# Kernel tuning notes

Measured on AMD Instinct MI355X. Metric: run time of the kernel, lower is better.

Reference implementation:

```python
import jax, jax.numpy as jnp
import numpy as np

TEMPERATURE = 8.0  # sqrt(dim_k=64)
NEG_INF = -1e30    # stand-in for -inf that stays finite-safe under softmax


def setup_inputs() -> dict:
    key = jax.random.key(0)
    kq, kk, kv, km = jax.random.split(key, 4)
    bsz, lq, lk, d = 64, 2048, 2048, 64
    q = jax.random.normal(kq, (bsz, lq, d), dtype=jnp.float32)
    k = jax.random.normal(kk, (bsz, lk, d), dtype=jnp.float32)
    v = jax.random.normal(kv, (bsz, lk, d), dtype=jnp.float32)
    mask = jax.random.normal(km, (bsz, lq, lk), dtype=jnp.float32)
    return {"q": q, "k": k, "v": v, "mask": mask}


def reference(q, k, v, mask):
    # attn = QK^T / temperature, additive graph mask, threshold -inf fill
    attn = jnp.einsum("bqd,bkd->bqk", q, k) / TEMPERATURE
    attn = attn + mask                       # graph_mask_type == 'add'
    attn = jnp.where(mask < 0, NEG_INF, attn)  # masked_fill(mask.lt(0), -inf)
    attn = jax.nn.softmax(attn, axis=2)
    # dropout p=0.0 -> identity
    output = jnp.einsum("bqk,bkd->bqd", attn, v)
    return (output, attn)
```

## Files before the change

kernel.cpp:

```cpp
#include <hip/hip_runtime.h>
#include <stdint.h>
#include <stddef.h>


typedef __attribute__((ext_vector_type(4))) float f32x4;
typedef __fp16 f16x2 __attribute__((ext_vector_type(2)));
typedef __fp16 f16x4 __attribute__((ext_vector_type(4)));
typedef __fp16 f16x8 __attribute__((ext_vector_type(8)));

static constexpr int BATCH = 64;
static constexpr int SEQ   = 2048;
static constexpr int HD    = 64;
static constexpr float NEGH = -60000.0f;

__global__ void frag_kernel(const float* __restrict__ k, const float* __restrict__ v,
                            __fp16* __restrict__ kf, __fp16* __restrict__ vf) {
  __shared__ float tile[64][68];
  if (blockIdx.x < 2048) {
    const int b    = blockIdx.x >> 5;
    const int ch   = blockIdx.x & 31;
    const int tid  = threadIdx.x;
    const int tl   = tid >> 6;
    const int lane = tid & 63;
    const int l15  = lane & 15;
    const int g    = lane >> 4;
    const int kt   = ch * 4 + tl;
    const float* src = k + ((size_t)(b * SEQ + kt * 16 + l15)) * HD + g * 8;
    char* dst = (char*)kf + ((size_t)(b * 128 + kt)) * 2048 + l15 * 64 + g * 16;
#pragma unroll
    for (int half = 0; half < 2; ++half) {
      f32x4 a = *(const f32x4*)(src + half * 32);
      f32x4 c = *(const f32x4*)(src + half * 32 + 4);
      f16x2 p0 = __builtin_amdgcn_cvt_pkrtz(a[0], a[1]);
      f16x2 p1 = __builtin_amdgcn_cvt_pkrtz(a[2], a[3]);
      f16x2 p2 = __builtin_amdgcn_cvt_pkrtz(c[0], c[1]);
      f16x2 p3 = __builtin_amdgcn_cvt_pkrtz(c[2], c[3]);
      f16x8 o;
      o[0] = p0[0]; o[1] = p0[1]; o[2] = p1[0]; o[3] = p1[1];
      o[4] = p2[0]; o[5] = p2[1]; o[6] = p3[0]; o[7] = p3[1];
      *(f16x8*)(dst + half * 1024) = o;
    }
  } else {
    const int bid = blockIdx.x - 2048;
    const int b   = bid >> 5;
    const int ch  = bid & 31;
    const int tid = threadIdx.x;
    const int kk  = tid >> 4;
    const int d4  = (tid & 15) << 2;
    const int k0  = ch * 64;
#pragma unroll
    for (int i = 0; i < 4; ++i) {
      f32x4 val = *(const f32x4*)(v + ((size_t)(b * SEQ + k0 + kk + 16 * i)) * HD + d4);
      tile[kk + 16 * i][d4 + 0] = val[0];
      tile[kk + 16 * i][d4 + 1] = val[1];
      tile[kk + 16 * i][d4 + 2] = val[2];
      tile[kk + 16 * i][d4 + 3] = val[3];
    }
    __syncthreads();
    const int tl  = tid >> 6;
    const int db  = (tid >> 4) & 3;
    const int l15 = tid & 15;
    f16x8 o0, o1;
#pragma unroll
    for (int g = 0; g < 2; ++g)
#pragma unroll
      for (int j = 0; j < 4; ++j)
        o0[g * 4 + j] = (__fp16)tile[tl * 16 + g * 4 + j][db * 16 + l15];
#pragma unroll
    for (int g = 0; g < 2; ++g)
#pragma unroll
      for (int j = 0; j < 4; ++j)
        o1[g * 4 + j] = (__fp16)tile[tl * 16 + (g + 2) * 4 + j][db * 16 + l15];
    char* dst = (char*)vf + ((size_t)(b * 128 + ch * 4 + tl)) * 2048 + db * 512 + l15 * 32;
    *(f16x8*)(dst)      = o0;
    *(f16x8*)(dst + 16) = o1;
  }
}

__global__ __launch_bounds__(256, 3) void attn_kernel(
    const float* __restrict__ q,
    const __fp16* __restrict__ kf,
    const __fp16* __restrict__ vf,
    const float* __restrict__ mask,
    float* __restrict__ out,
    float* __restrict__ attn) {
  __shared__ __align__(16) char pool[4][4352];
  __shared__ float stat_m[4][16];
  __shared__ float stat_l[4][16];

  const int tid  = threadIdx.x;
  const int w    = tid >> 6;
  const int lane = tid & 63;
  const int l15  = lane & 15;
  const int g    = lane >> 4;
  const int g4   = g << 2;

  const int bid = blockIdx.x;
  const int xcd = bid & 7;
  const int r   = bid >> 3;
  const int b   = xcd * 8 + (r >> 7);
  const int q0  = (r & 127) << 4;
  const int wk0 = w << 9;

  char* wb = pool[w];
  const int koff = l15 * 64 + g * 16;
  const int voff = l15 * 32 + g * 8;

  const char* kfb = (const char*)kf + ((size_t)(b * 128) + w * 32) * 2048;
  const char* vfb = (const char*)vf + ((size_t)(b * 128) + w * 32) * 2048;
  const float* mbase = mask + ((size_t)(b * SEQ + q0)) * SEQ + wk0;
  float*       abase = attn + ((size_t)(b * SEQ + q0)) * SEQ + wk0;

  f16x8 qb0, qb1;
  {
    const float* qsrc = q + ((size_t)(b * SEQ + q0 + l15)) * HD + g * 8;
    f32x4 a0 = *(const f32x4*)(qsrc);
    f32x4 a1 = *(const f32x4*)(qsrc + 4);
    f32x4 c0 = *(const f32x4*)(qsrc + 32);
    f32x4 c1 = *(const f32x4*)(qsrc + 36);
    f16x2 p0 = __builtin_amdgcn_cvt_pkrtz(a0[0], a0[1]);
    f16x2 p1 = __builtin_amdgcn_cvt_pkrtz(a0[2], a0[3]);
    f16x2 p2 = __builtin_amdgcn_cvt_pkrtz(a1[0], a1[1]);
    f16x2 p3 = __builtin_amdgcn_cvt_pkrtz(a1[2], a1[3]);
    qb0[0] = p0[0]; qb0[1] = p0[1]; qb0[2] = p1[0]; qb0[3] = p1[1];
    qb0[4] = p2[0]; qb0[5] = p2[1]; qb0[6] = p3[0]; qb0[7] = p3[1];
    p0 = __builtin_amdgcn_cvt_pkrtz(c0[0], c0[1]);
    p1 = __builtin_amdgcn_cvt_pkrtz(c0[2], c0[3]);
    p2 = __builtin_amdgcn_cvt_pkrtz(c1[0], c1[1]);
    p3 = __builtin_amdgcn_cvt_pkrtz(c1[2], c1[3]);
    qb1[0] = p0[0]; qb1[1] = p0[1]; qb1[2] = p1[0]; qb1[3] = p1[1];
    qb1[4] = p2[0]; qb1[5] = p2[1]; qb1[6] = p3[0]; qb1[7] = p3[1];
  }

  f16x4 PH0,  PH1,  PH2,  PH3,  PH4,  PH5,  PH6,  PH7;
  f16x4 PH8,  PH9,  PH10, PH11, PH12, PH13, PH14, PH15;
  f16x4 PH16, PH17, PH18, PH19, PH20, PH21, PH22, PH23;
  f16x4 PH24, PH25, PH26, PH27, PH28, PH29, PH30, PH31;

  f16x8 K0A, K0B, K1A, K1B, K2A, K2B, K3A, K3B;
  f32x4 MA0, MA1, MA2, MA3;
  f32x4 MB0, MB1, MB2, MB3;
  float m = -3.0e38f;

#define ISSUE_K(t, KA, KB)                                                   \
  KA = *(const f16x8*)(kfb + (size_t)(t) * 2048 + koff);                     \
  KB = *(const f16x8*)(kfb + (size_t)(t) * 2048 + 1024 + koff);

#define ISSUE_M(c, M0, M1, M2, M3)                                           \
  M0 = __builtin_nontemporal_load((const f32x4*)(mbase + (size_t)(0 * 4 + g) * SEQ + (c) * 64 + l15 * 4)); \
  M1 = __builtin_nontemporal_load((const f32x4*)(mbase + (size_t)(1 * 4 + g) * SEQ + (c) * 64 + l15 * 4)); \
  M2 = __builtin_nontemporal_load((const f32x4*)(mbase + (size_t)(2 * 4 + g) * SEQ + (c) * 64 + l15 * 4)); \
  M3 = __builtin_nontemporal_load((const f32x4*)(mbase + (size_t)(3 * 4 + g) * SEQ + (c) * 64 + l15 * 4));

#define WRITE_M(M0, M1, M2, M3)                                              \
  *(f32x4*)(wb + (0 * 4 + g) * 272 + l15 * 16) = M0;                         \
  *(f32x4*)(wb + (1 * 4 + g) * 272 + l15 * 16) = M1;                         \
  *(f32x4*)(wb + (2 * 4 + g) * 272 + l15 * 16) = M2;                         \
  *(f32x4*)(wb + (3 * 4 + g) * 272 + l15 * 16) = M3;

#define ATILE(t, PH, KA, KB)                                                 \
  {                                                                          \
    f32x4 acc = {0.f, 0.f, 0.f, 0.f};                                        \
    acc = __builtin_amdgcn_mfma_f32_16x16x32_f16(KA, qb0, acc, 0, 0, 0);     \
    acc = __builtin_amdgcn_mfma_f32_16x16x32_f16(KB, qb1, acc, 0, 0, 0);     \
    const f32x4 mv = *(const f32x4*)(wb + l15 * 272 + ((t) & 3) * 64 + g * 16); \
    float s0 = (mv[0] < 0.f) ? NEGH : fmaf(acc[0], 0.125f, mv[0]);           \
    float s1 = (mv[1] < 0.f) ? NEGH : fmaf(acc[1], 0.125f, mv[1]);           \
    float s2 = (mv[2] < 0.f) ? NEGH : fmaf(acc[2], 0.125f, mv[2]);           \
    float s3 = (mv[3] < 0.f) ? NEGH : fmaf(acc[3], 0.125f, mv[3]);           \
    m = fmaxf(m, fmaxf(fmaxf(s0, s1), fmaxf(s2, s3)));                       \
    f16x2 lo_ = __builtin_amdgcn_cvt_pkrtz(s0, s1);                          \
    f16x2 hi_ = __builtin_amdgcn_cvt_pkrtz(s2, s3);                          \
    PH = (f16x4){lo_[0], lo_[1], hi_[0], hi_[1]};                            \
  }

#define AT(t, PH, KA, KB)  ATILE(t, PH, KA, KB) ISSUE_K((t) + 4, KA, KB)
#define ATL(t, PH, KA, KB) ATILE(t, PH, KA, KB)

  ISSUE_M(0, MA0, MA1, MA2, MA3)
  ISSUE_K(0, K0A, K0B) ISSUE_K(1, K1A, K1B) ISSUE_K(2, K2A, K2B) ISSUE_K(3, K3A, K3B)
  ISSUE_M(1, MB0, MB1, MB2, MB3)

  WRITE_M(MA0, MA1, MA2, MA3) ISSUE_M(2, MA0, MA1, MA2, MA3)
  AT(0, PH0, K0A, K0B)  AT(1, PH1, K1A, K1B)  AT(2, PH2, K2A, K2B)  AT(3, PH3, K3A, K3B)
  WRITE_M(MB0, MB1, MB2, MB3) ISSUE_M(3, MB0, MB1, MB2, MB3)
  AT(4, PH4, K0A, K0B)  AT(5, PH5, K1A, K1B)  AT(6, PH6, K2A, K2B)  AT(7, PH7, K3A, K3B)
  WRITE_M(MA0, MA1, MA2, MA3) ISSUE_M(4, MA0, MA1, MA2, MA3)
  AT(8, PH8, K0A, K0B)  AT(9, PH9, K1A, K1B)  AT(10, PH10, K2A, K2B) AT(11, PH11, K3A, K3B)
  WRITE_M(MB0, MB1, MB2, MB3) ISSUE_M(5, MB0, MB1, MB2, MB3)
  AT(12, PH12, K0A, K0B) AT(13, PH13, K1A, K1B) AT(14, PH14, K2A, K2B) AT(15, PH15, K3A, K3B)
  WRITE_M(MA0, MA1, MA2, MA3) ISSUE_M(6, MA0, MA1, MA2, MA3)
  AT(16, PH16, K0A, K0B) AT(17, PH17, K1A, K1B) AT(18, PH18, K2A, K2B) AT(19, PH19, K3A, K3B)
  WRITE_M(MB0, MB1, MB2, MB3) ISSUE_M(7, MB0, MB1, MB2, MB3)
  AT(20, PH20, K0A, K0B) AT(21, PH21, K1A, K1B) AT(22, PH22, K2A, K2B) AT(23, PH23, K3A, K3B)
  WRITE_M(MA0, MA1, MA2, MA3)
  AT(24, PH24, K0A, K0B) AT(25, PH25, K1A, K1B) AT(26, PH26, K2A, K2B) AT(27, PH27, K3A, K3B)
  WRITE_M(MB0, MB1, MB2, MB3)
  ATL(28, PH28, K0A, K0B) ATL(29, PH29, K1A, K1B) ATL(30, PH30, K2A, K2B) ATL(31, PH31, K3A, K3B)

#undef AT
#undef ATL
#undef ATILE
#undef ISSUE_K
#undef ISSUE_M
#undef WRITE_M

  m = fmaxf(m, __shfl_xor(m, 16));
  m = fmaxf(m, __shfl_xor(m, 32));

  float lw = 0.f;
#define A2_STEP(PH)                                                          \
  {                                                                          \
    float e0 = __expf((float)PH[0] - m);                                     \
    float e1 = __expf((float)PH[1] - m);                                     \
    float e2 = __expf((float)PH[2] - m);                                     \
    float e3 = __expf((float)PH[3] - m);                                     \
    lw += (e0 + e1) + (e2 + e3);                                             \
    f16x2 lo_ = __builtin_amdgcn_cvt_pkrtz(e0, e1);                          \
    f16x2 hi_ = __builtin_amdgcn_cvt_pkrtz(e2, e3);                          \
    PH = (f16x4){lo_[0], lo_[1], hi_[0], hi_[1]};                            \
  }
  A2_STEP(PH0)  A2_STEP(PH1)  A2_STEP(PH2)  A2_STEP(PH3)
  A2_STEP(PH4)  A2_STEP(PH5)  A2_STEP(PH6)  A2_STEP(PH7)
  A2_STEP(PH8)  A2_STEP(PH9)  A2_STEP(PH10) A2_STEP(PH11)
  A2_STEP(PH12) A2_STEP(PH13) A2_STEP(PH14) A2_STEP(PH15)
  A2_STEP(PH16) A2_STEP(PH17) A2_STEP(PH18) A2_STEP(PH19)
  A2_STEP(PH20) A2_STEP(PH21) A2_STEP(PH22) A2_STEP(PH23)
  A2_STEP(PH24) A2_STEP(PH25) A2_STEP(PH26) A2_STEP(PH27)
  A2_STEP(PH28) A2_STEP(PH29) A2_STEP(PH30) A2_STEP(PH31)
#undef A2_STEP

  lw += __shfl_xor(lw, 16);
  lw += __shfl_xor(lw, 32);

  if (lane < 16) { stat_m[w][lane] = m; stat_l[w][lane] = lw; }
  __syncthreads();

  float mg = -3.0e38f;
#pragma unroll
  for (int ww = 0; ww < 4; ++ww) mg = fmaxf(mg, stat_m[ww][l15]);
  float lg = 0.f;
#pragma unroll
  for (int ww = 0; ww < 4; ++ww) lg += stat_l[ww][l15] * __expf(stat_m[ww][l15] - mg);
  const float scale = __expf(m - mg) / lg;
  const __fp16 hs = (__fp16)scale;
  const f16x4 sc4 = {hs, hs, hs, hs};

  f32x4 oacc0 = {0.f, 0.f, 0.f, 0.f};
  f32x4 oacc1 = {0.f, 0.f, 0.f, 0.f};
  f32x4 oacc2 = {0.f, 0.f, 0.f, 0.f};
  f32x4 oacc3 = {0.f, 0.f, 0.f, 0.f};

  f16x4 V0a, V0b, V0c, V0d, V1a, V1b, V1c, V1d;
  f16x4 V2a, V2b, V2c, V2d, V3a, V3b, V3c, V3d;

#define ISSUE_V(t, Va, Vb, Vc, Vd)                                           \
  Va = *(const f16x4*)(vfb + (size_t)(t) * 2048 + 0 * 512 + voff);           \
  Vb = *(const f16x4*)(vfb + (size_t)(t) * 2048 + 1 * 512 + voff);           \
  Vc = *(const f16x4*)(vfb + (size_t)(t) * 2048 + 2 * 512 + voff);           \
  Vd = *(const f16x4*)(vfb + (size_t)(t) * 2048 + 3 * 512 + voff);

#define BTILE(t, PH, Va, Vb, Vc, Vd)                                         \
  {                                                                          \
    const f16x4 pf = PH * sc4;                                               \
    f32x4 st;                                                                \
    st[0] = (float)pf[0]; st[1] = (float)pf[1];                              \
    st[2] = (float)pf[2]; st[3] = (float)pf[3];                              \
    *(f32x4*)(wb + l15 * 272 + ((t) & 3) * 64 + g * 16) = st;                \
    oacc0 = __builtin_amdgcn_mfma_f32_16x16x16f16(Va, pf, oacc0, 0, 0, 0);   \
    oacc1 = __builtin_amdgcn_mfma_f32_16x16x16f16(Vb, pf, oacc1, 0, 0, 0);   \
    oacc2 = __builtin_amdgcn_mfma_f32_16x16x16f16(Vc, pf, oacc2, 0, 0, 0);   \
    oacc3 = __builtin_amdgcn_mfma_f32_16x16x16f16(Vd, pf, oacc3, 0, 0, 0);   \
  }

#define STORE_A(c)                                                           \
  __builtin_nontemporal_store(                                               \
      *(const f32x4*)(wb + (0 * 4 + g) * 272 + l15 * 16),                    \
      (f32x4*)(abase + (size_t)(0 * 4 + g) * SEQ + (c) * 64 + l15 * 4));     \
  __builtin_nontemporal_store(                                               \
      *(const f32x4*)(wb + (1 * 4 + g) * 272 + l15 * 16),                    \
      (f32x4*)(abase + (size_t)(1 * 4 + g) * SEQ + (c) * 64 + l15 * 4));     \
  __builtin_nontemporal_store(                                               \
      *(const f32x4*)(wb + (2 * 4 + g) * 272 + l15 * 16),                    \
      (f32x4*)(abase + (size_t)(2 * 4 + g) * SEQ + (c) * 64 + l15 * 4));     \
  __builtin_nontemporal_store(                                               \
      *(const f32x4*)(wb + (3 * 4 + g) * 272 + l15 * 16),                    \
      (f32x4*)(abase + (size_t)(3 * 4 + g) * SEQ + (c) * 64 + l15 * 4));

#define BS(t, PH, Va, Vb, Vc, Vd)  BTILE(t, PH, Va, Vb, Vc, Vd) ISSUE_V((t) + 4, Va, Vb, Vc, Vd)
#define BSL(t, PH, Va, Vb, Vc, Vd) BTILE(t, PH, Va, Vb, Vc, Vd)

  ISSUE_V(0, V0a, V0b, V0c, V0d) ISSUE_V(1, V1a, V1b, V1c, V1d)
  ISSUE_V(2, V2a, V2b, V2c, V2d) ISSUE_V(3, V3a, V3b, V3c, V3d)

  BS(0, PH0, V0a, V0b, V0c, V0d)   BS(1, PH1, V1a, V1b, V1c, V1d)
  BS(2, PH2, V2a, V2b, V2c, V2d)   BS(3, PH3, V3a, V3b, V3c, V3d)   STORE_A(0)
  BS(4, PH4, V0a, V0b, V0c, V0d)   BS(5, PH5, V1a, V1b, V1c, V1d)
  BS(6, PH6, V2a, V2b, V2c, V2d)   BS(7, PH7, V3a, V3b, V3c, V3d)   STORE_A(1)
  BS(8, PH8, V0a, V0b, V0c, V0d)   BS(9, PH9, V1a, V1b, V1c, V1d)
  BS(10, PH10, V2a, V2b, V2c, V2d) BS(11, PH11, V3a, V3b, V3c, V3d) STORE_A(2)
  BS(12, PH12, V0a, V0b, V0c, V0d) BS(13, PH13, V1a, V1b, V1c, V1d)
  BS(14, PH14, V2a, V2b, V2c, V2d) BS(15, PH15, V3a, V3b, V3c, V3d) STORE_A(3)
  BS(16, PH16, V0a, V0b, V0c, V0d) BS(17, PH17, V1a, V1b, V1c, V1d)
  BS(18, PH18, V2a, V2b, V2c, V2d) BS(19, PH19, V3a, V3b, V3c, V3d) STORE_A(4)
  BS(20, PH20, V0a, V0b, V0c, V0d) BS(21, PH21, V1a, V1b, V1c, V1d)
  BS(22, PH22, V2a, V2b, V2c, V2d) BS(23, PH23, V3a, V3b, V3c, V3d) STORE_A(5)
  BS(24, PH24, V0a, V0b, V0c, V0d) BS(25, PH25, V1a, V1b, V1c, V1d)
  BS(26, PH26, V2a, V2b, V2c, V2d) BS(27, PH27, V3a, V3b, V3c, V3d) STORE_A(6)
  BSL(28, PH28, V0a, V0b, V0c, V0d) BSL(29, PH29, V1a, V1b, V1c, V1d)
  BSL(30, PH30, V2a, V2b, V2c, V2d) BSL(31, PH31, V3a, V3b, V3c, V3d) STORE_A(7)

#undef BS
#undef BSL
#undef BTILE
#undef ISSUE_V
#undef STORE_A

  float* sred_w = (float*)pool[w];
#pragma unroll
  for (int rr = 0; rr < 4; ++rr) {
    sred_w[(0 * 16 + g4 + rr) * 17 + l15] = oacc0[rr];
    sred_w[(1 * 16 + g4 + rr) * 17 + l15] = oacc1[rr];
    sred_w[(2 * 16 + g4 + rr) * 17 + l15] = oacc2[rr];
    sred_w[(3 * 16 + g4 + rr) * 17 + l15] = oacc3[rr];
  }
  __syncthreads();

#pragma unroll
  for (int ii = 0; ii < 4; ++ii) {
    const int i = tid + ii * 256;
    const int qq = i >> 6;
    const int d = i & 63;
    const int o = d * 17 + qq;
    float s = ((const float*)pool[0])[o] + ((const float*)pool[1])[o] +
              ((const float*)pool[2])[o] + ((const float*)pool[3])[o];
    out[((size_t)(b * SEQ + q0 + qq)) * HD + d] = s;
  }
}

extern "C" void kernel_launch(void* const* d_in, const int* in_sizes, int n_in,
                              void* d_out, int out_size, void* d_ws, size_t ws_size,
                              hipStream_t stream) {
  const float* q    = (const float*)d_in[0];
  const float* k    = (const float*)d_in[1];
  const float* v    = (const float*)d_in[2];
  const float* mask = (const float*)d_in[3];

  float* out  = (float*)d_out;
  float* attn = out + (size_t)BATCH * SEQ * HD;

  const size_t nqk = (size_t)BATCH * SEQ * HD;
  __fp16* kfrag = (__fp16*)d_ws;
  __fp16* vfrag = kfrag + nqk;

  frag_kernel<<<dim3(2 * BATCH * 32), dim3(256), 0, stream>>>(k, v, kfrag, vfrag);
  attn_kernel<<<dim3(BATCH * (SEQ / 16)), dim3(256), 0, stream>>>(q, kfrag, vfrag, mask, out, attn);
}
```

Before: 518.5 us.

## Split key dimension across eight waves per block instead of four

Doubles the block to 512 threads so each of eight waves handles 256 keys instead of 512. Per-wave register tiles (PH arrays) are halved, which lowers register pressure and lets more waves run per CU (launch bounds 512,4). In exchange the cross-wave softmax statistics and output reduction span eight partitions, and each wave's mask/K/V prefetch pipeline is shorter, giving less latency hiding per wave.

```diff
diff --git a/kernel.cpp b/kernel.cpp
--- a/kernel.cpp
+++ b/kernel.cpp
@@ -77,16 +77,16 @@
   }
 }
 
-__global__ __launch_bounds__(256, 3) void attn_kernel(
+__global__ __launch_bounds__(512, 4) void attn_kernel(
     const float* __restrict__ q,
     const __fp16* __restrict__ kf,
     const __fp16* __restrict__ vf,
     const float* __restrict__ mask,
     float* __restrict__ out,
     float* __restrict__ attn) {
-  __shared__ __align__(16) char pool[4][4352];
-  __shared__ float stat_m[4][16];
-  __shared__ float stat_l[4][16];
+  __shared__ __align__(16) char pool[8][4352];
+  __shared__ float stat_m[8][16];
+  __shared__ float stat_l[8][16];
 
   const int tid  = threadIdx.x;
   const int w    = tid >> 6;
@@ -100,14 +100,14 @@
   const int r   = bid >> 3;
   const int b   = xcd * 8 + (r >> 7);
   const int q0  = (r & 127) << 4;
-  const int wk0 = w << 9;
+  const int wk0 = w << 8;
 
   char* wb = pool[w];
   const int koff = l15 * 64 + g * 16;
   const int voff = l15 * 32 + g * 8;
 
-  const char* kfb = (const char*)kf + ((size_t)(b * 128) + w * 32) * 2048;
-  const char* vfb = (const char*)vf + ((size_t)(b * 128) + w * 32) * 2048;
+  const char* kfb = (const char*)kf + ((size_t)(b * 128) + w * 16) * 2048;
+  const char* vfb = (const char*)vf + ((size_t)(b * 128) + w * 16) * 2048;
   const float* mbase = mask + ((size_t)(b * SEQ + q0)) * SEQ + wk0;
   float*       abase = attn + ((size_t)(b * SEQ + q0)) * SEQ + wk0;
 
@@ -134,8 +134,6 @@
 
   f16x4 PH0,  PH1,  PH2,  PH3,  PH4,  PH5,  PH6,  PH7;
   f16x4 PH8,  PH9,  PH10, PH11, PH12, PH13, PH14, PH15;
-  f16x4 PH16, PH17, PH18, PH19, PH20, PH21, PH22, PH23;
-  f16x4 PH24, PH25, PH26, PH27, PH28, PH29, PH30, PH31;
 
   f16x8 K0A, K0B, K1A, K1B, K2A, K2B, K3A, K3B;
   f32x4 MA0, MA1, MA2, MA3;
@@ -185,18 +183,10 @@
   AT(0, PH0, K0A, K0B)  AT(1, PH1, K1A, K1B)  AT(2, PH2, K2A, K2B)  AT(3, PH3, K3A, K3B)
   WRITE_M(MB0, MB1, MB2, MB3) ISSUE_M(3, MB0, MB1, MB2, MB3)
   AT(4, PH4, K0A, K0B)  AT(5, PH5, K1A, K1B)  AT(6, PH6, K2A, K2B)  AT(7, PH7, K3A, K3B)
-  WRITE_M(MA0, MA1, MA2, MA3) ISSUE_M(4, MA0, MA1, MA2, MA3)
+  WRITE_M(MA0, MA1, MA2, MA3)
   AT(8, PH8, K0A, K0B)  AT(9, PH9, K1A, K1B)  AT(10, PH10, K2A, K2B) AT(11, PH11, K3A, K3B)
-  WRITE_M(MB0, MB1, MB2, MB3) ISSUE_M(5, MB0, MB1, MB2, MB3)
-  AT(12, PH12, K0A, K0B) AT(13, PH13, K1A, K1B) AT(14, PH14, K2A, K2B) AT(15, PH15, K3A, K3B)
-  WRITE_M(MA0, MA1, MA2, MA3) ISSUE_M(6, MA0, MA1, MA2, MA3)
-  AT(16, PH16, K0A, K0B) AT(17, PH17, K1A, K1B) AT(18, PH18, K2A, K2B) AT(19, PH19, K3A, K3B)
-  WRITE_M(MB0, MB1, MB2, MB3) ISSUE_M(7, MB0, MB1, MB2, MB3)
-  AT(20, PH20, K0A, K0B) AT(21, PH21, K1A, K1B) AT(22, PH22, K2A, K2B) AT(23, PH23, K3A, K3B)
-  WRITE_M(MA0, MA1, MA2, MA3)
-  AT(24, PH24, K0A, K0B) AT(25, PH25, K1A, K1B) AT(26, PH26, K2A, K2B) AT(27, PH27, K3A, K3B)
   WRITE_M(MB0, MB1, MB2, MB3)
-  ATL(28, PH28, K0A, K0B) ATL(29, PH29, K1A, K1B) ATL(30, PH30, K2A, K2B) ATL(31, PH31, K3A, K3B)
+  ATL(12, PH12, K0A, K0B) ATL(13, PH13, K1A, K1B) ATL(14, PH14, K2A, K2B) ATL(15, PH15, K3A, K3B)
 
 #undef AT
 #undef ATL
@@ -224,10 +214,6 @@
   A2_STEP(PH4)  A2_STEP(PH5)  A2_STEP(PH6)  A2_STEP(PH7)
   A2_STEP(PH8)  A2_STEP(PH9)  A2_STEP(PH10) A2_STEP(PH11)
   A2_STEP(PH12) A2_STEP(PH13) A2_STEP(PH14) A2_STEP(PH15)
-  A2_STEP(PH16) A2_STEP(PH17) A2_STEP(PH18) A2_STEP(PH19)
-  A2_STEP(PH20) A2_STEP(PH21) A2_STEP(PH22) A2_STEP(PH23)
-  A2_STEP(PH24) A2_STEP(PH25) A2_STEP(PH26) A2_STEP(PH27)
-  A2_STEP(PH28) A2_STEP(PH29) A2_STEP(PH30) A2_STEP(PH31)
 #undef A2_STEP
 
   lw += __shfl_xor(lw, 16);
@@ -238,10 +224,10 @@
 
   float mg = -3.0e38f;
 #pragma unroll
-  for (int ww = 0; ww < 4; ++ww) mg = fmaxf(mg, stat_m[ww][l15]);
+  for (int ww = 0; ww < 8; ++ww) mg = fmaxf(mg, stat_m[ww][l15]);
   float lg = 0.f;
 #pragma unroll
-  for (int ww = 0; ww < 4; ++ww) lg += stat_l[ww][l15] * __expf(stat_m[ww][l15] - mg);
+  for (int ww = 0; ww < 8; ++ww) lg += stat_l[ww][l15] * __expf(stat_m[ww][l15] - mg);
   const float scale = __expf(m - mg) / lg;
   const __fp16 hs = (__fp16)scale;
   const f16x4 sc4 = {hs, hs, hs, hs};
@@ -299,16 +285,8 @@
   BS(6, PH6, V2a, V2b, V2c, V2d)   BS(7, PH7, V3a, V3b, V3c, V3d)   STORE_A(1)
   BS(8, PH8, V0a, V0b, V0c, V0d)   BS(9, PH9, V1a, V1b, V1c, V1d)
   BS(10, PH10, V2a, V2b, V2c, V2d) BS(11, PH11, V3a, V3b, V3c, V3d) STORE_A(2)
-  BS(12, PH12, V0a, V0b, V0c, V0d) BS(13, PH13, V1a, V1b, V1c, V1d)
-  BS(14, PH14, V2a, V2b, V2c, V2d) BS(15, PH15, V3a, V3b, V3c, V3d) STORE_A(3)
-  BS(16, PH16, V0a, V0b, V0c, V0d) BS(17, PH17, V1a, V1b, V1c, V1d)
-  BS(18, PH18, V2a, V2b, V2c, V2d) BS(19, PH19, V3a, V3b, V3c, V3d) STORE_A(4)
-  BS(20, PH20, V0a, V0b, V0c, V0d) BS(21, PH21, V1a, V1b, V1c, V1d)
-  BS(22, PH22, V2a, V2b, V2c, V2d) BS(23, PH23, V3a, V3b, V3c, V3d) STORE_A(5)
-  BS(24, PH24, V0a, V0b, V0c, V0d) BS(25, PH25, V1a, V1b, V1c, V1d)
-  BS(26, PH26, V2a, V2b, V2c, V2d) BS(27, PH27, V3a, V3b, V3c, V3d) STORE_A(6)
-  BSL(28, PH28, V0a, V0b, V0c, V0d) BSL(29, PH29, V1a, V1b, V1c, V1d)
-  BSL(30, PH30, V2a, V2b, V2c, V2d) BSL(31, PH31, V3a, V3b, V3c, V3d) STORE_A(7)
+  BSL(12, PH12, V0a, V0b, V0c, V0d) BSL(13, PH13, V1a, V1b, V1c, V1d)
+  BSL(14, PH14, V2a, V2b, V2c, V2d) BSL(15, PH15, V3a, V3b, V3c, V3d) STORE_A(3)
 
 #undef BS
 #undef BSL
@@ -327,13 +305,14 @@
   __syncthreads();
 
 #pragma unroll
-  for (int ii = 0; ii < 4; ++ii) {
-    const int i = tid + ii * 256;
+  for (int ii = 0; ii < 2; ++ii) {
+    const int i = tid + ii * 512;
     const int qq = i >> 6;
     const int d = i & 63;
     const int o = d * 17 + qq;
-    float s = ((const float*)pool[0])[o] + ((const float*)pool[1])[o] +
-              ((const float*)pool[2])[o] + ((const float*)pool[3])[o];
+    float s = 0.f;
+#pragma unroll
+    for (int ww = 0; ww < 8; ++ww) s += ((const float*)pool[ww])[o];
     out[((size_t)(b * SEQ + q0 + qq)) * HD + d] = s;
   }
 }
@@ -354,5 +333,5 @@
   __fp16* vfrag = kfrag + nqk;
 
   frag_kernel<<<dim3(2 * BATCH * 32), dim3(256), 0, stream>>>(k, v, kfrag, vfrag);
-  attn_kernel<<<dim3(BATCH * (SEQ / 16)), dim3(256), 0, stream>>>(q, kfrag, vfrag, mask, out, attn);
+  attn_kernel<<<dim3(BATCH * (SEQ / 16)), dim3(512), 0, stream>>>(q, kfrag, vfrag, mask, out, attn);
 }
```

New measurement: 613.3 us. +18.3%, slower.
